# Performance work log

Hardware: AMD Instinct MI355X
Metric: run time of the kernel (lower is better)

Reference implementation:

```python
import jax, jax.numpy as jnp
import numpy as np

CUTOFF = 5.0
N, F, NRBF, E = 20000, 128, 20, 320000


def _init_linear(key, fan_in, fan_out):
    kw, kb = jax.random.split(key)
    lim = 1.0 / np.sqrt(fan_in)
    W = jax.random.uniform(kw, (fan_in, fan_out), minval=-lim, maxval=lim, dtype=jnp.float32)
    b = jax.random.uniform(kb, (fan_out,), minval=-lim, maxval=lim, dtype=jnp.float32)
    return W, b


def setup_inputs() -> dict:
    key = jax.random.key(0)
    ks = jax.random.split(key, 16)
    s = jax.random.normal(ks[0], (N, F), dtype=jnp.float32)
    v = jax.random.normal(ks[1], (N, F, 3), dtype=jnp.float32)
    rbf = jax.random.uniform(ks[2], (E, NRBF), dtype=jnp.float32)
    r_ij_direction = jax.random.normal(ks[3], (E, 3), dtype=jnp.float32)
    r_ij_direction = r_ij_direction / jnp.linalg.norm(r_ij_direction, axis=-1, keepdims=True)
    i_index = jax.random.randint(ks[4], (E,), 0, N)
    j_index = jax.random.randint(ks[5], (E,), 0, N)
    W1, b1 = _init_linear(ks[6], F, F)
    W2, b2 = _init_linear(ks[7], F, 3 * F)
    Wr, br = _init_linear(ks[8], NRBF, 3 * F)
    WU, bU = _init_linear(ks[9], F, F)
    WV, bV = _init_linear(ks[10], F, F)
    M1, bm1 = _init_linear(ks[11], 2 * F, F)
    M2, bm2 = _init_linear(ks[12], F, 3 * F)
    return dict(s=s, v=v, rbf=rbf, r_ij_direction=r_ij_direction,
                W1=W1, b1=b1, W2=W2, b2=b2, Wr=Wr, br=br,
                WU=WU, bU=bU, WV=WV, bV=bV, M1=M1, bm1=bm1, M2=M2, bm2=bm2,
                i_index=i_index, j_index=j_index)


def reference(s, v, rbf, r_ij_direction, W1, b1, W2, b2, Wr, br,
              WU, bU, WV, bV, M1, bm1, M2, bm2, i_index, j_index):
    silu = jax.nn.silu
    nf = s.shape[1]
    # message: gather j, small MLP on scalar features -> [E, 3F]
    phi = silu(s[j_index] @ W1 + b1) @ W2 + b2
    # rbf filter, passed elementwise through the cosine cutoff (faithful to source)
    x = rbf @ Wr + br
    W = 0.5 * (jnp.cos(x * jnp.pi / CUTOFF) + 1.0) * (x < CUTOFF).astype(x.dtype)
    split = phi * W
    Ws, Wvs, Wvv = split[:, :nf], split[:, nf:2 * nf], split[:, 2 * nf:]
    # vector messages: [E, F, 3]
    delta_v_all = Wvs[:, :, None] * r_ij_direction[:, None, :] + Wvv[:, :, None] * v[j_index]
    v = v + jnp.zeros_like(v).at[i_index].add(delta_v_all)
    s = s + jnp.zeros_like(s).at[i_index].add(Ws)
    # update block: linear maps over feature axis of [N, F, 3] vectors
    Uv = jnp.einsum('nfd,fg->ngd', v, WU) + bU[None, :, None]
    Vv = jnp.einsum('nfd,fg->ngd', v, WV) + bV[None, :, None]
    Vv_norm = jnp.linalg.norm(Vv, axis=2)  # [N, F]
    mlp_in = jnp.concatenate([Vv_norm, s], axis=-1)  # [N, 2F]
    m = silu(mlp_in @ M1 + bm1) @ M2 + bm2  # [N, 3F]
    a_vv, a_sv, a_ss = m[:, :nf], m[:, nf:2 * nf], m[:, 2 * nf:]
    dv = a_vv[:, :, None] * Uv
    ds = jnp.sum(Uv * Vv, axis=2) * a_sv + a_ss
    return (s + ds, v + dv)
```

## Files before the change

### kernel.cpp

```cpp
#include <hip/hip_runtime.h>
#include <hip/hip_bf16.h>
#include <math.h>

#define N_NODES 20000
#define F 128
#define NRBF 20
#define E_EDGES 320000
#define F3 (3 * F)
#define NCHUNK ((N_NODES + 255) / 256)

typedef __attribute__((ext_vector_type(8))) short bf16x8;
typedef __attribute__((ext_vector_type(4))) float f32x4;

__device__ __forceinline__ float silu_f(float x) {
    return x / (1.0f + __expf(-x));
}
__device__ __forceinline__ unsigned short bf_bits(float x) {
    __hip_bfloat16 b = __float2bfloat16(x);
    return *(unsigned short*)&b;
}
__device__ __forceinline__ void bf_split(float x, unsigned short& hi, unsigned short& lo) {
    __hip_bfloat16 h = __float2bfloat16(x);
    float hf = __bfloat162float(h);
    __hip_bfloat16 l = __float2bfloat16(x - hf);
    hi = *(unsigned short*)&h;
    lo = *(unsigned short*)&l;
}

__global__ __launch_bounds__(256) void w_swizzle_all(
    const float* __restrict__ W1, const float* __restrict__ W2,
    const float* __restrict__ WU, const float* __restrict__ WV,
    const float* __restrict__ M1, const float* __restrict__ M2,
    unsigned short* __restrict__ W1s, unsigned short* __restrict__ W2s,
    unsigned short* __restrict__ WUVs, unsigned short* __restrict__ M1s,
    unsigned short* __restrict__ M2s)
{
    int tid = blockIdx.x * 256 + threadIdx.x;
    if (tid < 8 * 4 * 64) {
        int lane = tid & 63, kc = (tid >> 6) & 3, ct = tid >> 8;
        int n = ct * 16 + (lane & 15);
        int k0 = kc * 32 + (lane >> 4) * 8;
        #pragma unroll
        for (int j = 0; j < 8; ++j)
            W1s[tid * 8 + j] = bf_bits(W1[(k0 + j) * F + n]);
    } else if (tid < 8 * 4 * 64 + 24 * 4 * 64) {
        int t = tid - 8 * 4 * 64;
        int lane = t & 63, kc = (t >> 6) & 3, ct = t >> 8;
        int n = ct * 16 + (lane & 15);
        int k0 = kc * 32 + (lane >> 4) * 8;
        #pragma unroll
        for (int j = 0; j < 8; ++j)
            W2s[t * 8 + j] = bf_bits(W2[(k0 + j) * F3 + n]);
    } else if (tid < 8192 + 224 * 64) {
        int t2 = tid - 8192;
        int lane = t2 & 63;
        int set = t2 >> 6;
        if (set < 64) {
            int kc = set & 3, ct = set >> 2;
            int n = ct * 16 + (lane & 15);
            int k0 = kc * 32 + (lane >> 4) * 8;
            const float* W = (ct < 8) ? WU : WV;
            int nn = n & 127;
            #pragma unroll
            for (int j = 0; j < 8; ++j)
                WUVs[(size_t)(set * 64 + lane) * 8 + j] = bf_bits(W[(k0 + j) * F + nn]);
        } else if (set < 128) {
            int t = set - 64;
            int kc = t & 7, ct = t >> 3;
            int n = ct * 16 + (lane & 15);
            int k0 = kc * 32 + (lane >> 4) * 8;
            #pragma unroll
            for (int j = 0; j < 8; ++j)
                M1s[(size_t)(t * 64 + lane) * 8 + j] = bf_bits(M1[(k0 + j) * F + n]);
        } else {
            int t = set - 128;
            int kc = t & 3, ct = t >> 2;
            int n = ct * 16 + (lane & 15);
            int k0 = kc * 32 + (lane >> 4) * 8;
            #pragma unroll
            for (int j = 0; j < 8; ++j)
                M2s[(size_t)(t * 64 + lane) * 8 + j] = bf_bits(M2[(k0 + j) * F3 + n]);
        }
    }
}

#define SLD 136
__global__ __launch_bounds__(256) void node_mlp_mfma(
    const float* __restrict__ s, const float* __restrict__ b1,
    const float* __restrict__ b2,
    const unsigned short* __restrict__ W1s, const unsigned short* __restrict__ W2s,
    float* __restrict__ h)
{
    __shared__ unsigned short Sl[64][SLD];
    __shared__ unsigned short Hid[4][16][SLD];

    const int tid = threadIdx.x;
    const int lane = tid & 63, wave = tid >> 6;
    const int m = lane & 15, quad = lane >> 4;
    const int n0 = blockIdx.x * 64;

    for (int i = tid; i < 64 * F; i += 256) {
        int r = i >> 7, c = i & 127;
        int nn = n0 + r;
        if (nn >= N_NODES) nn = N_NODES - 1;
        Sl[r][c] = bf_bits(s[(size_t)nn * F + c]);
    }
    __syncthreads();

    const int arow = wave * 16 + m;
    bf16x8 a1[4];
    #pragma unroll
    for (int kc = 0; kc < 4; ++kc)
        a1[kc] = *(const bf16x8*)&Sl[arow][kc * 32 + quad * 8];

    const bf16x8* W1f = (const bf16x8*)W1s;
    #pragma unroll
    for (int ct = 0; ct < 8; ++ct) {
        f32x4 acc = {0.f, 0.f, 0.f, 0.f};
        #pragma unroll
        for (int kc = 0; kc < 4; ++kc)
            acc = __builtin_amdgcn_mfma_f32_16x16x32_bf16(
                a1[kc], W1f[(ct * 4 + kc) * 64 + lane], acc, 0, 0, 0);
        float bias = b1[ct * 16 + m];
        #pragma unroll
        for (int r = 0; r < 4; ++r)
            Hid[wave][quad * 4 + r][ct * 16 + m] = bf_bits(silu_f(acc[r] + bias));
    }
    __syncthreads();

    bf16x8 a2[4];
    #pragma unroll
    for (int kc = 0; kc < 4; ++kc)
        a2[kc] = *(const bf16x8*)&Hid[wave][m][kc * 32 + quad * 8];

    const bf16x8* W2f = (const bf16x8*)W2s;
    #pragma unroll
    for (int ct = 0; ct < 24; ++ct) {
        f32x4 acc = {0.f, 0.f, 0.f, 0.f};
        #pragma unroll
        for (int kc = 0; kc < 4; ++kc)
            acc = __builtin_amdgcn_mfma_f32_16x16x32_bf16(
                a2[kc], W2f[(ct * 4 + kc) * 64 + lane], acc, 0, 0, 0);
        float bias = b2[ct * 16 + m];
        #pragma unroll
        for (int r = 0; r < 4; ++r) {
            int node = n0 + wave * 16 + quad * 4 + r;
            if (node < N_NODES)
                h[(size_t)node * F3 + ct * 16 + m] = acc[r] + bias;
        }
    }
}

__global__ __launch_bounds__(256) void hist_kernel(const int* __restrict__ i_index,
                                                   int* __restrict__ counts)
{
    int e = blockIdx.x * 256 + threadIdx.x;
    if (e < E_EDGES) atomicAdd(&counts[i_index[e]], 1);
}

__global__ __launch_bounds__(256) void scan_p1(const int* __restrict__ counts,
                                               int* __restrict__ row_start,
                                               int* __restrict__ chunk_sum)
{
    __shared__ int buf[256];
    const int tid = threadIdx.x;
    const int idx = blockIdx.x * 256 + tid;
    int val = (idx < N_NODES) ? counts[idx] : 0;
    buf[tid] = val;
    __syncthreads();
    for (int off = 1; off < 256; off <<= 1) {
        int t = (tid >= off) ? buf[tid - off] : 0;
        __syncthreads();
        buf[tid] += t;
        __syncthreads();
    }
    if (idx < N_NODES) row_start[idx] = buf[tid] - val;
    if (tid == 255) chunk_sum[blockIdx.x] = buf[255];
}

__global__ __launch_bounds__(128) void scan_p2(const int* __restrict__ chunk_sum,
                                               int* __restrict__ chunk_off)
{
    __shared__ int buf[128];
    const int tid = threadIdx.x;
    int val = (tid < NCHUNK) ? chunk_sum[tid] : 0;
    buf[tid] = val;
    __syncthreads();
    for (int off = 1; off < 128; off <<= 1) {
        int t = (tid >= off) ? buf[tid - off] : 0;
        __syncthreads();
        buf[tid] += t;
        __syncthreads();
    }
    if (tid < NCHUNK) chunk_off[tid] = buf[tid] - val;
}

__global__ __launch_bounds__(256) void scan_p3(int* __restrict__ row_start,
                                               const int* __restrict__ chunk_off,
                                               int* __restrict__ cursor)
{
    int idx = blockIdx.x * 256 + threadIdx.x;
    if (idx < N_NODES) {
        int vv = row_start[idx] + chunk_off[blockIdx.x];
        row_start[idx] = vv;
        cursor[idx] = vv;
    }
    if (idx == 0) row_start[N_NODES] = E_EDGES;
}

__global__ __launch_bounds__(256) void scatter_kernel(const int* __restrict__ i_index,
                                                      const int* __restrict__ j_index,
                                                      const float* __restrict__ dir,
                                                      int* __restrict__ cursor,
                                                      int* __restrict__ edge_ids,
                                                      int* __restrict__ edge_j,
                                                      float* __restrict__ edge_dir4)
{
    int e = blockIdx.x * 256 + threadIdx.x;
    if (e < E_EDGES) {
        int j = j_index[e];
        float dx = dir[(size_t)e * 3 + 0];
        float dy = dir[(size_t)e * 3 + 1];
        float dz = dir[(size_t)e * 3 + 2];
        int pos = atomicAdd(&cursor[i_index[e]], 1);
        edge_ids[pos] = e;
        edge_j[pos] = j;
        f32x4 d4 = {dx, dy, dz, 0.0f};
        *(f32x4*)(edge_dir4 + (size_t)pos * 4) = d4;
    }
}

__global__ __launch_bounds__(256) void agg_kernel(
    const float* __restrict__ s, const float* __restrict__ v,
    const float* __restrict__ rbf,
    const float* __restrict__ Wr, const float* __restrict__ br,
    const float* __restrict__ h,
    const int* __restrict__ row_start, const int* __restrict__ edge_ids,
    const int* __restrict__ edge_j, const float* __restrict__ edge_dir4,
    float* __restrict__ s_agg, float* __restrict__ v_agg)
{
    const int tid = threadIdx.x;
    const int n = blockIdx.x;
    const int beg = row_start[n];
    const int end = row_start[n + 1];
    const float cc = 0.6283185307179586f;

    if (tid < 128) {
        const int f = tid;
        float wr0[NRBF];
        #pragma unroll
        for (int k = 0; k < NRBF; ++k)
            wr0[k] = Wr[k * F3 + f];
        const float br0 = br[f];

        float s_acc = s[n * F + f];

        for (int idx = beg; idx < end; ++idx) {
            const int e = edge_ids[idx];
            const int j = edge_j[idx];

            float x0 = br0;
            #pragma unroll
            for (int k = 0; k < NRBF; ++k)
                x0 += rbf[e * NRBF + k] * wr0[k];
            float w0 = (x0 < 5.0f) ? 0.5f * (__cosf(x0 * cc) + 1.0f) : 0.0f;

            s_acc += h[j * F3 + f] * w0;
        }
        s_agg[n * F + f] = s_acc;
    } else {
        const int f = tid - 128;
        float wr1[NRBF], wr2[NRBF];
        #pragma unroll
        for (int k = 0; k < NRBF; ++k) {
            wr1[k] = Wr[k * F3 + F + f];
            wr2[k] = Wr[k * F3 + 2 * F + f];
        }
        const float br1 = br[F + f], br2 = br[2 * F + f];

        float v0 = v[n * F3 + f * 3 + 0];
        float v1 = v[n * F3 + f * 3 + 1];
        float v2 = v[n * F3 + f * 3 + 2];

        for (int idx = beg; idx < end; ++idx) {
            const int e = edge_ids[idx];
            const int j = edge_j[idx];

            float x1 = br1, x2 = br2;
            #pragma unroll
            for (int k = 0; k < NRBF; ++k) {
                float r = rbf[e * NRBF + k];
                x1 += r * wr1[k];
                x2 += r * wr2[k];
            }
            float w1 = (x1 < 5.0f) ? 0.5f * (__cosf(x1 * cc) + 1.0f) : 0.0f;
            float w2 = (x2 < 5.0f) ? 0.5f * (__cosf(x2 * cc) + 1.0f) : 0.0f;

            float hvs = h[j * F3 + F + f]     * w1;
            float hvv = h[j * F3 + 2 * F + f] * w2;

            float dx = edge_dir4[idx * 4 + 0];
            float dy = edge_dir4[idx * 4 + 1];
            float dz = edge_dir4[idx * 4 + 2];

            float vj0 = v[j * F3 + f * 3 + 0];
            float vj1 = v[j * F3 + f * 3 + 1];
            float vj2 = v[j * F3 + f * 3 + 2];

            v0 += hvs * dx + hvv * vj0;
            v1 += hvs * dy + hvv * vj1;
            v2 += hvs * dz + hvv * vj2;
        }
        v_agg[n * F3 + f * 3 + 0] = v0;
        v_agg[n * F3 + f * 3 + 1] = v1;
        v_agg[n * F3 + f * 3 + 2] = v2;
    }
}

#define UB 16
__global__ __launch_bounds__(256) void update_mfma(
    const float* __restrict__ s_agg, const float* __restrict__ v_agg,
    const unsigned short* __restrict__ WUVs,
    const float* __restrict__ bU, const float* __restrict__ bV,
    const unsigned short* __restrict__ M1s, const float* __restrict__ bm1,
    const unsigned short* __restrict__ M2s, const float* __restrict__ bm2,
    float* __restrict__ s_out, float* __restrict__ v_out)
{
    __shared__ unsigned short VAh[48][SLD],  VAl[48][SLD];
    __shared__ unsigned short MIh[16][264],  MIl[16][264];
    __shared__ unsigned short HIh[16][SLD],  HIl[16][SLD];

    const int tid = threadIdx.x;
    const int lane = tid & 63, wave = tid >> 6;
    const int m = lane & 15, quad = lane >> 4;
    const int n0 = blockIdx.x * UB;

    for (int i = tid; i < UB * F3; i += 256) {
        int nl = i / F3, r = i - nl * F3;
        int f = r / 3, d = r - f * 3;
        unsigned short hi, lo;
        bf_split(v_agg[(size_t)n0 * F3 + i], hi, lo);
        VAh[d * 16 + nl][f] = hi;
        VAl[d * 16 + nl][f] = lo;
    }
    __syncthreads();

    f32x4 accU[3][2], accV[3][2];
    #pragma unroll
    for (int d = 0; d < 3; ++d)
        #pragma unroll
        for (int c = 0; c < 2; ++c) {
            accU[d][c] = (f32x4){0.f, 0.f, 0.f, 0.f};
            accV[d][c] = (f32x4){0.f, 0.f, 0.f, 0.f};
        }

    const bf16x8* Wf  = (const bf16x8*)WUVs;
    #pragma unroll
    for (int kc = 0; kc < 4; ++kc) {
        bf16x8 bu0 = Wf[((wave * 2 + 0) * 4 + kc) * 64 + lane];
        bf16x8 bu1 = Wf[((wave * 2 + 1) * 4 + kc) * 64 + lane];
        bf16x8 bv0 = Wf[((8 + wave * 2 + 0) * 4 + kc) * 64 + lane];
        bf16x8 bv1 = Wf[((8 + wave * 2 + 1) * 4 + kc) * 64 + lane];
        #pragma unroll
        for (int d = 0; d < 3; ++d) {
            bf16x8 ah = *(const bf16x8*)&VAh[d * 16 + m][kc * 32 + quad * 8];
            bf16x8 al = *(const bf16x8*)&VAl[d * 16 + m][kc * 32 + quad * 8];
            accU[d][0] = __builtin_amdgcn_mfma_f32_16x16x32_bf16(ah, bu0, accU[d][0], 0, 0, 0);
            accU[d][0] = __builtin_amdgcn_mfma_f32_16x16x32_bf16(al, bu0, accU[d][0], 0, 0, 0);
            accU[d][1] = __builtin_amdgcn_mfma_f32_16x16x32_bf16(ah, bu1, accU[d][1], 0, 0, 0);
            accU[d][1] = __builtin_amdgcn_mfma_f32_16x16x32_bf16(al, bu1, accU[d][1], 0, 0, 0);
            accV[d][0] = __builtin_amdgcn_mfma_f32_16x16x32_bf16(ah, bv0, accV[d][0], 0, 0, 0);
            accV[d][0] = __builtin_amdgcn_mfma_f32_16x16x32_bf16(al, bv0, accV[d][0], 0, 0, 0);
            accV[d][1] = __builtin_amdgcn_mfma_f32_16x16x32_bf16(ah, bv1, accV[d][1], 0, 0, 0);
            accV[d][1] = __builtin_amdgcn_mfma_f32_16x16x32_bf16(al, bv1, accV[d][1], 0, 0, 0);
        }
    }

    #pragma unroll
    for (int c = 0; c < 2; ++c) {
        int g = wave * 32 + c * 16 + m;
        float bu = bU[g], bv = bV[g];
        #pragma unroll
        for (int d = 0; d < 3; ++d)
            #pragma unroll
            for (int r = 0; r < 4; ++r) {
                accU[d][c][r] += bu;
                accV[d][c][r] += bv;
            }
        #pragma unroll
        for (int r = 0; r < 4; ++r) {
            int nl = quad * 4 + r;
            float nv = sqrtf(accV[0][c][r] * accV[0][c][r] +
                             accV[1][c][r] * accV[1][c][r] +
                             accV[2][c][r] * accV[2][c][r]);
            unsigned short hi, lo;
            bf_split(nv, hi, lo);
            MIh[nl][g] = hi; MIl[nl][g] = lo;
            bf_split(s_agg[(size_t)(n0 + nl) * F + g], hi, lo);
            MIh[nl][128 + g] = hi; MIl[nl][128 + g] = lo;
        }
    }
    __syncthreads();

    f32x4 acc2[2];
    acc2[0] = (f32x4){0.f, 0.f, 0.f, 0.f};
    acc2[1] = (f32x4){0.f, 0.f, 0.f, 0.f};
    const bf16x8* M1f = (const bf16x8*)M1s;
    #pragma unroll
    for (int kc = 0; kc < 8; ++kc) {
        bf16x8 ah = *(const bf16x8*)&MIh[m][kc * 32 + quad * 8];
        bf16x8 al = *(const bf16x8*)&MIl[m][kc * 32 + quad * 8];
        bf16x8 b0 = M1f[((wave * 2 + 0) * 8 + kc) * 64 + lane];
        bf16x8 b1 = M1f[((wave * 2 + 1) * 8 + kc) * 64 + lane];
        acc2[0] = __builtin_amdgcn_mfma_f32_16x16x32_bf16(ah, b0, acc2[0], 0, 0, 0);
        acc2[0] = __builtin_amdgcn_mfma_f32_16x16x32_bf16(al, b0, acc2[0], 0, 0, 0);
        acc2[1] = __builtin_amdgcn_mfma_f32_16x16x32_bf16(ah, b1, acc2[1], 0, 0, 0);
        acc2[1] = __builtin_amdgcn_mfma_f32_16x16x32_bf16(al, b1, acc2[1], 0, 0, 0);
    }
    #pragma unroll
    for (int c = 0; c < 2; ++c) {
        int g = wave * 32 + c * 16 + m;
        float bh = bm1[g];
        #pragma unroll
        for (int r = 0; r < 4; ++r) {
            unsigned short hi, lo;
            bf_split(silu_f(acc2[c][r] + bh), hi, lo);
            HIh[quad * 4 + r][g] = hi;
            HIl[quad * 4 + r][g] = lo;
        }
    }
    __syncthreads();

    f32x4 acc3[3][2];
    #pragma unroll
    for (int o = 0; o < 3; ++o)
        #pragma unroll
        for (int c = 0; c < 2; ++c)
            acc3[o][c] = (f32x4){0.f, 0.f, 0.f, 0.f};
    const bf16x8* M2f = (const bf16x8*)M2s;
    #pragma unroll
    for (int kc = 0; kc < 4; ++kc) {
        bf16x8 ah = *(const bf16x8*)&HIh[m][kc * 32 + quad * 8];
        bf16x8 al = *(const bf16x8*)&HIl[m][kc * 32 + quad * 8];
        #pragma unroll
        for (int o = 0; o < 3; ++o)
            #pragma unroll
            for (int c = 0; c < 2; ++c) {
                bf16x8 bb = M2f[(((o * 8) + wave * 2 + c) * 4 + kc) * 64 + lane];
                acc3[o][c] = __builtin_amdgcn_mfma_f32_16x16x32_bf16(ah, bb, acc3[o][c], 0, 0, 0);
                acc3[o][c] = __builtin_amdgcn_mfma_f32_16x16x32_bf16(al, bb, acc3[o][c], 0, 0, 0);
            }
    }

    #pragma unroll
    for (int c = 0; c < 2; ++c) {
        int g = wave * 32 + c * 16 + m;
        float bvv = bm2[g], bsv = bm2[128 + g], bss = bm2[256 + g];
        #pragma unroll
        for (int r = 0; r < 4; ++r) {
            int nl = quad * 4 + r;
            int n = n0 + nl;
            float a_vv = acc3[0][c][r] + bvv;
            float a_sv = acc3[1][c][r] + bsv;
            float a_ss = acc3[2][c][r] + bss;
            float dotuv = accU[0][c][r] * accV[0][c][r] +
                          accU[1][c][r] * accV[1][c][r] +
                          accU[2][c][r] * accV[2][c][r];
            s_out[(size_t)n * F + g] =
                s_agg[(size_t)n * F + g] + dotuv * a_sv + a_ss;
            #pragma unroll
            for (int d = 0; d < 3; ++d)
                v_out[(size_t)n * F3 + g * 3 + d] =
                    v_agg[(size_t)n * F3 + g * 3 + d] + a_vv * accU[d][c][r];
        }
    }
}

extern "C" void kernel_launch(void* const* d_in, const int* in_sizes, int n_in,
                              void* d_out, int out_size, void* d_ws, size_t ws_size,
                              hipStream_t stream) {
    const float* s    = (const float*)d_in[0];
    const float* v    = (const float*)d_in[1];
    const float* rbf  = (const float*)d_in[2];
    const float* dir  = (const float*)d_in[3];
    const float* W1   = (const float*)d_in[4];
    const float* b1   = (const float*)d_in[5];
    const float* W2   = (const float*)d_in[6];
    const float* b2   = (const float*)d_in[7];
    const float* Wr   = (const float*)d_in[8];
    const float* br   = (const float*)d_in[9];
    const float* WU   = (const float*)d_in[10];
    const float* bU   = (const float*)d_in[11];
    const float* WV   = (const float*)d_in[12];
    const float* bV   = (const float*)d_in[13];
    const float* M1   = (const float*)d_in[14];
    const float* bm1  = (const float*)d_in[15];
    const float* M2   = (const float*)d_in[16];
    const float* bm2  = (const float*)d_in[17];
    const int* i_index = (const int*)d_in[18];
    const int* j_index = (const int*)d_in[19];

    float* out_s = (float*)d_out;
    float* out_v = out_s + (size_t)N_NODES * F;

    float* h       = (float*)d_ws;
    float* s_agg   = h + (size_t)N_NODES * F3;
    float* v_agg   = s_agg + (size_t)N_NODES * F;
    float* edge_dir4 = v_agg + (size_t)N_NODES * F3;
    int*   counts  = (int*)(edge_dir4 + (size_t)E_EDGES * 4);
    int*   row_start = counts + N_NODES;
    int*   cursor  = row_start + N_NODES + 1;
    int*   edge_ids = cursor + N_NODES;
    int*   edge_j  = edge_ids + E_EDGES;
    int*   chunk_sum = edge_j + E_EDGES;
    int*   chunk_off = chunk_sum + 128;
    unsigned short* W1s = (unsigned short*)(chunk_off + 128);
    unsigned short* W2s = W1s + 8 * 4 * 64 * 8;
    unsigned short* WUVs = W2s + 24 * 4 * 64 * 8;
    unsigned short* M1s  = WUVs + 16 * 4 * 64 * 8;
    unsigned short* M2s  = M1s + 8 * 8 * 64 * 8;

    hipMemsetAsync(counts, 0, sizeof(int) * N_NODES, stream);

    w_swizzle_all<<<88, 256, 0, stream>>>(W1, W2, WU, WV, M1, M2,
                                          W1s, W2s, WUVs, M1s, M2s);
    node_mlp_mfma<<<(N_NODES + 63) / 64, 256, 0, stream>>>(s, b1, b2, W1s, W2s, h);

    hist_kernel<<<(E_EDGES + 255) / 256, 256, 0, stream>>>(i_index, counts);
    scan_p1<<<NCHUNK, 256, 0, stream>>>(counts, row_start, chunk_sum);
    scan_p2<<<1, 128, 0, stream>>>(chunk_sum, chunk_off);
    scan_p3<<<NCHUNK, 256, 0, stream>>>(row_start, chunk_off, cursor);
    scatter_kernel<<<(E_EDGES + 255) / 256, 256, 0, stream>>>(i_index, j_index, dir,
                                                              cursor, edge_ids, edge_j,
                                                              edge_dir4);

    agg_kernel<<<N_NODES, 256, 0, stream>>>(s, v, rbf, Wr, br, h,
                                            row_start, edge_ids, edge_j, edge_dir4,
                                            s_agg, v_agg);

    update_mfma<<<N_NODES / UB, 256, 0, stream>>>(s_agg, v_agg, WUVs, bU, bV,
                                                  M1s, bm1, M2s, bm2, out_s, out_v);
}
```

Baseline: 399.7 us.

## Compute per-edge RBF filter with split-bf16 MFMA into shared memory

Replaces the per-thread scalar 20-term dot products of rbf with Wr (redundantly recomputed by every feature thread) with batched 16-edge MFMA tiles using hi/lo bf16 splitting for near-fp32 accuracy. The cosine cutoff filter is written to an LDS tile and then consumed by the aggregation loops. This removes the per-edge scalar FMAs and the repeated rbf loads across threads. In exchange it adds block-level syncs per 16-edge batch and an extra pre-swizzle of Wr. Nodes average about 16 edges, so the MFMA tiles are mostly full.

Result: slower. 472.4 us (+18.2%).

```diff
diff --git a/kernel.cpp b/kernel.cpp
--- a/kernel.cpp
+++ b/kernel.cpp
@@ -31,9 +31,11 @@
     const float* __restrict__ W1, const float* __restrict__ W2,
     const float* __restrict__ WU, const float* __restrict__ WV,
     const float* __restrict__ M1, const float* __restrict__ M2,
+    const float* __restrict__ Wr,
     unsigned short* __restrict__ W1s, unsigned short* __restrict__ W2s,
     unsigned short* __restrict__ WUVs, unsigned short* __restrict__ M1s,
-    unsigned short* __restrict__ M2s)
+    unsigned short* __restrict__ M2s,
+    unsigned short* __restrict__ WrHs, unsigned short* __restrict__ WrLs)
 {
     int tid = blockIdx.x * 256 + threadIdx.x;
     if (tid < 8 * 4 * 64) {
@@ -81,6 +83,21 @@
             for (int j = 0; j < 8; ++j)
                 M2s[(size_t)(t * 64 + lane) * 8 + j] = bf_bits(M2[(k0 + j) * F3 + n]);
         }
+    } else if (tid < 8192 + 14336 + 1536) {
+        int t3 = tid - (8192 + 14336);
+        int lane = t3 & 63;
+        int ct = t3 >> 6;
+        int n = ct * 16 + (lane & 15);
+        int k0 = (lane >> 4) * 8;
+        #pragma unroll
+        for (int j = 0; j < 8; ++j) {
+            int k = k0 + j;
+            float val = (k < NRBF) ? Wr[k * F3 + n] : 0.0f;
+            unsigned short hi, lo;
+            bf_split(val, hi, lo);
+            WrHs[(size_t)(ct * 64 + lane) * 8 + j] = hi;
+            WrLs[(size_t)(ct * 64 + lane) * 8 + j] = lo;
+        }
     }
 }
 
@@ -233,87 +250,112 @@
 __global__ __launch_bounds__(256) void agg_kernel(
     const float* __restrict__ s, const float* __restrict__ v,
     const float* __restrict__ rbf,
-    const float* __restrict__ Wr, const float* __restrict__ br,
-    const float* __restrict__ h,
+    const unsigned short* __restrict__ WrHs, const unsigned short* __restrict__ WrLs,
+    const float* __restrict__ br, const float* __restrict__ h,
     const int* __restrict__ row_start, const int* __restrict__ edge_ids,
     const int* __restrict__ edge_j, const float* __restrict__ edge_dir4,
     float* __restrict__ s_agg, float* __restrict__ v_agg)
 {
+    __shared__ float Wlds[16][396];
+
     const int tid = threadIdx.x;
+    const int lane = tid & 63, wave = tid >> 6;
+    const int m = lane & 15, quad = lane >> 4;
     const int n = blockIdx.x;
     const int beg = row_start[n];
     const int end = row_start[n + 1];
     const float cc = 0.6283185307179586f;
 
+    float br6[6];
+    #pragma unroll
+    for (int t = 0; t < 6; ++t)
+        br6[t] = br[(wave * 6 + t) * 16 + m];
+
+    const int f = tid & 127;
+    float a0, a1, a2;
     if (tid < 128) {
-        const int f = tid;
-        float wr0[NRBF];
-        #pragma unroll
-        for (int k = 0; k < NRBF; ++k)
-            wr0[k] = Wr[k * F3 + f];
-        const float br0 = br[f];
-
-        float s_acc = s[n * F + f];
-
-        for (int idx = beg; idx < end; ++idx) {
-            const int e = edge_ids[idx];
-            const int j = edge_j[idx];
-
-            float x0 = br0;
-            #pragma unroll
-            for (int k = 0; k < NRBF; ++k)
-                x0 += rbf[e * NRBF + k] * wr0[k];
-            float w0 = (x0 < 5.0f) ? 0.5f * (__cosf(x0 * cc) + 1.0f) : 0.0f;
-
-            s_acc += h[j * F3 + f] * w0;
-        }
-        s_agg[n * F + f] = s_acc;
+        a0 = s[n * F + f];
+        a1 = 0.0f; a2 = 0.0f;
     } else {
-        const int f = tid - 128;
-        float wr1[NRBF], wr2[NRBF];
-        #pragma unroll
-        for (int k = 0; k < NRBF; ++k) {
-            wr1[k] = Wr[k * F3 + F + f];
-            wr2[k] = Wr[k * F3 + 2 * F + f];
-        }
-        const float br1 = br[F + f], br2 = br[2 * F + f];
-
-        float v0 = v[n * F3 + f * 3 + 0];
-        float v1 = v[n * F3 + f * 3 + 1];
-        float v2 = v[n * F3 + f * 3 + 2];
-
-        for (int idx = beg; idx < end; ++idx) {
-            const int e = edge_ids[idx];
-            const int j = edge_j[idx];
-
-            float x1 = br1, x2 = br2;
-            #pragma unroll
-            for (int k = 0; k < NRBF; ++k) {
-                float r = rbf[e * NRBF + k];
-                x1 += r * wr1[k];
-                x2 += r * wr2[k];
+        a0 = v[n * F3 + f * 3 + 0];
+        a1 = v[n * F3 + f * 3 + 1];
+        a2 = v[n * F3 + f * 3 + 2];
+    }
+
+    const bf16x8* WrHf = (const bf16x8*)WrHs;
+    const bf16x8* WrLf = (const bf16x8*)WrLs;
+
+    for (int base = beg; base < end; base += 16) {
+        bf16x8 ah, al;
+        #pragma unroll
+        for (int j = 0; j < 8; ++j) { ah[j] = 0; al[j] = 0; }
+        const int eidx = base + m;
+        if (eidx < end) {
+            const int e = edge_ids[eidx];
+            #pragma unroll
+            for (int j = 0; j < 8; ++j) {
+                int k = quad * 8 + j;
+                if (k < NRBF) {
+                    unsigned short hi, lo;
+                    bf_split(rbf[e * NRBF + k], hi, lo);
+                    ah[j] = (short)hi;
+                    al[j] = (short)lo;
+                }
             }
-            float w1 = (x1 < 5.0f) ? 0.5f * (__cosf(x1 * cc) + 1.0f) : 0.0f;
-            float w2 = (x2 < 5.0f) ? 0.5f * (__cosf(x2 * cc) + 1.0f) : 0.0f;
-
-            float hvs = h[j * F3 + F + f]     * w1;
-            float hvv = h[j * F3 + 2 * F + f] * w2;
-
-            float dx = edge_dir4[idx * 4 + 0];
-            float dy = edge_dir4[idx * 4 + 1];
-            float dz = edge_dir4[idx * 4 + 2];
-
-            float vj0 = v[j * F3 + f * 3 + 0];
-            float vj1 = v[j * F3 + f * 3 + 1];
-            float vj2 = v[j * F3 + f * 3 + 2];
-
-            v0 += hvs * dx + hvv * vj0;
-            v1 += hvs * dy + hvv * vj1;
-            v2 += hvs * dz + hvv * vj2;
-        }
-        v_agg[n * F3 + f * 3 + 0] = v0;
-        v_agg[n * F3 + f * 3 + 1] = v1;
-        v_agg[n * F3 + f * 3 + 2] = v2;
+        }
+
+        #pragma unroll
+        for (int t = 0; t < 6; ++t) {
+            const int ct = wave * 6 + t;
+            bf16x8 bh = WrHf[ct * 64 + lane];
+            bf16x8 bl = WrLf[ct * 64 + lane];
+            f32x4 acc = {0.f, 0.f, 0.f, 0.f};
+            acc = __builtin_amdgcn_mfma_f32_16x16x32_bf16(ah, bh, acc, 0, 0, 0);
+            acc = __builtin_amdgcn_mfma_f32_16x16x32_bf16(al, bh, acc, 0, 0, 0);
+            acc = __builtin_amdgcn_mfma_f32_16x16x32_bf16(ah, bl, acc, 0, 0, 0);
+            #pragma unroll
+            for (int r = 0; r < 4; ++r) {
+                float x = acc[r] + br6[t];
+                Wlds[quad * 4 + r][ct * 16 + m] =
+                    (x < 5.0f) ? 0.5f * (__cosf(x * cc) + 1.0f) : 0.0f;
+            }
+        }
+        __syncthreads();
+
+        const int nb = (end - base < 16) ? (end - base) : 16;
+        if (tid < 128) {
+            for (int t = 0; t < nb; ++t) {
+                const int j = edge_j[base + t];
+                a0 += h[j * F3 + f] * Wlds[t][f];
+            }
+        } else {
+            for (int t = 0; t < nb; ++t) {
+                const int idx = base + t;
+                const int j = edge_j[idx];
+                float w1 = Wlds[t][F + f];
+                float w2 = Wlds[t][2 * F + f];
+                float hvs = h[j * F3 + F + f]     * w1;
+                float hvv = h[j * F3 + 2 * F + f] * w2;
+                float dx = edge_dir4[idx * 4 + 0];
+                float dy = edge_dir4[idx * 4 + 1];
+                float dz = edge_dir4[idx * 4 + 2];
+                float vj0 = v[j * F3 + f * 3 + 0];
+                float vj1 = v[j * F3 + f * 3 + 1];
+                float vj2 = v[j * F3 + f * 3 + 2];
+                a0 += hvs * dx + hvv * vj0;
+                a1 += hvs * dy + hvv * vj1;
+                a2 += hvs * dz + hvv * vj2;
+            }
+        }
+        __syncthreads();
+    }
+
+    if (tid < 128) {
+        s_agg[n * F + f] = a0;
+    } else {
+        v_agg[n * F3 + f * 3 + 0] = a0;
+        v_agg[n * F3 + f * 3 + 1] = a1;
+        v_agg[n * F3 + f * 3 + 2] = a2;
     }
 }
 
@@ -519,11 +561,13 @@
     unsigned short* WUVs = W2s + 24 * 4 * 64 * 8;
     unsigned short* M1s  = WUVs + 16 * 4 * 64 * 8;
     unsigned short* M2s  = M1s + 8 * 8 * 64 * 8;
+    unsigned short* WrHs = M2s + 24 * 4 * 64 * 8;
+    unsigned short* WrLs = WrHs + 24 * 64 * 8;
 
     hipMemsetAsync(counts, 0, sizeof(int) * N_NODES, stream);
 
-    w_swizzle_all<<<88, 256, 0, stream>>>(W1, W2, WU, WV, M1, M2,
-                                          W1s, W2s, WUVs, M1s, M2s);
+    w_swizzle_all<<<94, 256, 0, stream>>>(W1, W2, WU, WV, M1, M2, Wr,
+                                          W1s, W2s, WUVs, M1s, M2s, WrHs, WrLs);
     node_mlp_mfma<<<(N_NODES + 63) / 64, 256, 0, stream>>>(s, b1, b2, W1s, W2s, h);
 
     hist_kernel<<<(E_EDGES + 255) / 256, 256, 0, stream>>>(i_index, counts);
@@ -534,7 +578,7 @@
                                                               cursor, edge_ids, edge_j,
                                                               edge_dir4);
 
-    agg_kernel<<<N_NODES, 256, 0, stream>>>(s, v, rbf, Wr, br, h,
+    agg_kernel<<<N_NODES, 256, 0, stream>>>(s, v, rbf, WrHs, WrLs, br, h,
                                             row_start, edge_ids, edge_j, edge_dir4,
                                             s_agg, v_agg);
 
```
